# Kernel tuning notes

Hardware: AMD Instinct MI355X
Metric: run time of the kernel (lower is better)

Reference implementation:

```python
import jax, jax.numpy as jnp
import numpy as np

D_MODEL = 1024
D_STATE = 16
BATCH = 16384
LN_EPS = 1e-5


def _linear_params(key, out_d, in_d):
    # torch nn.Linear default init: U(-1/sqrt(in_d), 1/sqrt(in_d))
    bound = 1.0 / np.sqrt(in_d)
    kw, kb = jax.random.split(key)
    W = jax.random.uniform(kw, (out_d, in_d), minval=-bound, maxval=bound, dtype=jnp.float32)
    b = jax.random.uniform(kb, (out_d,), minval=-bound, maxval=bound, dtype=jnp.float32)
    return W, b


def setup_inputs() -> dict:
    key = jax.random.key(0)
    k_x, k_b, k_c, k_dt, k_o = jax.random.split(key, 5)
    Wb, bb = _linear_params(k_b, D_STATE, D_MODEL)
    Wc, bc = _linear_params(k_c, D_STATE, D_MODEL)
    Wdt, bdt = _linear_params(k_dt, D_MODEL, D_MODEL)
    Wo, bo = _linear_params(k_o, D_MODEL, D_MODEL)
    return {
        "x": jax.random.normal(k_x, (BATCH, D_MODEL), dtype=jnp.float32),
        "gamma": jnp.ones((D_MODEL,), jnp.float32),   # LayerNorm weight
        "beta": jnp.zeros((D_MODEL,), jnp.float32),   # LayerNorm bias
        "Wb": Wb, "bb": bb,
        "Wc": Wc, "bc": bc,
        "Wdt": Wdt, "bdt": bdt,
        "D_skip": jnp.ones((D_MODEL,), jnp.float32),  # self.D parameter
        "Wo": Wo, "bo": bo,
    }


def reference(x, gamma, beta, Wb, bb, Wc, bc, Wdt, bdt, D_skip, Wo, bo):
    residual = x
    # LayerNorm
    mu = jnp.mean(x, axis=-1, keepdims=True)
    var = jnp.var(x, axis=-1, keepdims=True)
    xn = (x - mu) * jax.lax.rsqrt(var + LN_EPS) * gamma + beta  # (B, D)

    Bm = xn @ Wb.T + bb                     # (B, N)
    Cm = xn @ Wc.T + bc                     # (B, N)
    dt = jax.nn.softplus(xn @ Wdt.T + bdt)  # (B, D)
    # dA = exp(dt[...,None] * -exp(A_log)) is computed in the original but unused.

    # h = dt[:,:,None] * Bm[:,None,:] * xn[:,:,None]; y = (h * Cm[:,None,:]).sum(-1)
    # The N-reduction factors: sum_n Bm[b,n]*Cm[b,n] is d-independent.
    s = jnp.sum(Bm * Cm, axis=-1, keepdims=True)  # (B, 1)
    y = dt * xn * s + xn * D_skip                 # (B, D)

    y = y @ Wo.T + bo
    return y + residual  # dropout is identity at inference
```

## Files before the change

### kernel.cpp

```cpp
#include <hip/hip_runtime.h>
#include <math.h>

#define BATCH   16384
#define DMODEL  1024
#define KPACK   3072
#define KPHYS   2048
#define LN_EPS  1e-5f

typedef __bf16 bf16x8 __attribute__((ext_vector_type(8)));
typedef float  f32x4  __attribute__((ext_vector_type(4)));

static __device__ __forceinline__ unsigned short f2bf(float v) {
  union { float f; unsigned u; } c; c.f = v;
  unsigned r = c.u + 0x7fffu + ((c.u >> 16) & 1u);
  return (unsigned short)(r >> 16);
}
static __device__ __forceinline__ float bf2f(unsigned short h) {
  union { unsigned u; float f; } c; c.u = ((unsigned)h) << 16;
  return c.f;
}

static __device__ __forceinline__ void gload16(const void* g, void* l) {
  __builtin_amdgcn_global_load_lds(
      (const __attribute__((address_space(1))) void*)g,
      (__attribute__((address_space(3))) void*)l, 16, 0, 0);
}

#define S_BAR() __builtin_amdgcn_s_barrier()
#define LGKM0() do { asm volatile("s_waitcnt lgkmcnt(0)" ::: "memory"); \
                     __builtin_amdgcn_sched_barrier(0); } while (0)
#define VMC8()  do { asm volatile("s_waitcnt vmcnt(8)" ::: "memory"); \
                     __builtin_amdgcn_sched_barrier(0); } while (0)

__global__ __launch_bounds__(256) void pack_kernel(
    const float* __restrict__ Wdt, const float* __restrict__ Wo,
    const float* __restrict__ Wb, const float* __restrict__ Wc,
    unsigned short* __restrict__ WdtP, unsigned short* __restrict__ WoP,
    unsigned short* __restrict__ WbcP) {
  int r = blockIdx.x;
  const float* src;
  unsigned short* dst;
  if (r < 1024)      { src = Wdt + (size_t)r * 1024;        dst = WdtP + (size_t)r * KPHYS; }
  else if (r < 2048) { src = Wo  + (size_t)(r-1024) * 1024; dst = WoP  + (size_t)(r-1024) * KPHYS; }
  else if (r < 2064) { src = Wb  + (size_t)(r-2048) * 1024; dst = WbcP + (size_t)(r-2048) * KPHYS; }
  else               { src = Wc  + (size_t)(r-2064) * 1024; dst = WbcP + (size_t)(r-2064+16) * KPHYS; }
  int t = threadIdx.x;
  float4 v = ((const float4*)src)[t];
  ushort4 hs, ls; unsigned short h;
  h = f2bf(v.x); hs.x = h; ls.x = f2bf(v.x - bf2f(h));
  h = f2bf(v.y); hs.y = h; ls.y = f2bf(v.y - bf2f(h));
  h = f2bf(v.z); hs.z = h; ls.z = f2bf(v.z - bf2f(h));
  h = f2bf(v.w); hs.w = h; ls.w = f2bf(v.w - bf2f(h));
  ((ushort4*)dst)[t] = hs;
  ((ushort4*)(dst + 1024))[t] = ls;
}

__global__ __launch_bounds__(256) void ln_kernel(
    const float* __restrict__ x, const float* __restrict__ gamma,
    const float* __restrict__ beta, unsigned short* __restrict__ xnp) {
  const int row = blockIdx.x;
  const int tid = threadIdx.x;
  const float4* xr = (const float4*)(x + (size_t)row * DMODEL);
  float4 v = xr[tid];
  float s = v.x + v.y + v.z + v.w;
  float q = v.x * v.x + v.y * v.y + v.z * v.z + v.w * v.w;
#pragma unroll
  for (int m = 1; m < 64; m <<= 1) {
    s += __shfl_xor(s, m, 64);
    q += __shfl_xor(q, m, 64);
  }
  __shared__ float ws[4], wq[4];
  int w = tid >> 6, l = tid & 63;
  if (l == 0) { ws[w] = s; wq[w] = q; }
  __syncthreads();
  s = ws[0] + ws[1] + ws[2] + ws[3];
  q = wq[0] + wq[1] + wq[2] + wq[3];
  float mu = s * (1.0f / DMODEL);
  float var = q * (1.0f / DMODEL) - mu * mu;
  float rs = rsqrtf(var + LN_EPS);
  float4 g = ((const float4*)gamma)[tid];
  float4 b = ((const float4*)beta)[tid];
  float xn0 = (v.x - mu) * rs * g.x + b.x;
  float xn1 = (v.y - mu) * rs * g.y + b.y;
  float xn2 = (v.z - mu) * rs * g.z + b.z;
  float xn3 = (v.w - mu) * rs * g.w + b.w;
  ushort4 hs, ls; unsigned short h;
  h = f2bf(xn0); hs.x = h; ls.x = f2bf(xn0 - bf2f(h));
  h = f2bf(xn1); hs.y = h; ls.y = f2bf(xn1 - bf2f(h));
  h = f2bf(xn2); hs.z = h; ls.z = f2bf(xn2 - bf2f(h));
  h = f2bf(xn3); hs.w = h; ls.w = f2bf(xn3 - bf2f(h));
  unsigned short* dst = xnp + (size_t)row * KPHYS;
  ((ushort4*)dst)[tid] = hs;
  ((ushort4*)(dst + 1024))[tid] = ls;
}

__global__ __launch_bounds__(256) void bc_kernel(
    const unsigned short* __restrict__ XNP, const unsigned short* __restrict__ WbcP,
    const float* __restrict__ bb, const float* __restrict__ bcv, float* __restrict__ S) {
  __shared__ char smem[(64 + 32) * 128];
  char* sA = smem;
  char* sB = smem + 64 * 128;
  const int tid = threadIdx.x;
  const int l = tid & 63;
  const int w = tid >> 6;
  const int m0 = blockIdx.x * 64;
  f32x4 acc0 = {0.f, 0.f, 0.f, 0.f};
  f32x4 acc1 = {0.f, 0.f, 0.f, 0.f};
  for (int kt = 0; kt < KPACK; kt += 64) {
    int ksA = kt < 2048 ? kt : kt - 2048;
    int ksB = kt < 1024 ? kt : kt - 1024;
#pragma unroll
    for (int i = 0; i < 2; ++i) {
      int qq = i * 256 + tid;
      int row = qq >> 3, ch = qq & 7;
      gload16(XNP + (size_t)(m0 + row) * KPHYS + ksA + ((ch ^ (row & 7)) << 3),
              sA + (i * 256 + w * 64) * 16);
    }
    {
      int row = tid >> 3, ch = tid & 7;
      gload16(WbcP + (size_t)row * KPHYS + ksB + ((ch ^ (row & 7)) << 3),
              sB + (w * 64) * 16);
    }
    __syncthreads();
#pragma unroll
    for (int kk = 0; kk < 2; ++kk) {
      int cs = ((kk * 4 + (l >> 4)) ^ (l & 7)) * 16;
      bf16x8 a  = *(const bf16x8*)(sA + (w * 16 + (l & 15)) * 128 + cs);
      bf16x8 b0 = *(const bf16x8*)(sB + ((l & 15)) * 128 + cs);
      bf16x8 b1 = *(const bf16x8*)(sB + (16 + (l & 15)) * 128 + cs);
      acc0 = __builtin_amdgcn_mfma_f32_16x16x32_bf16(a, b0, acc0, 0, 0, 0);
      acc1 = __builtin_amdgcn_mfma_f32_16x16x32_bf16(a, b1, acc1, 0, 0, 0);
    }
    __syncthreads();
  }
  int c = l & 15;
#pragma unroll
  for (int j = 0; j < 4; ++j) {
    float bmv = acc0[j] + bb[c];
    float cmv = acc1[j] + bcv[c];
    float p = bmv * cmv;
    p += __shfl_xor(p, 1, 64);
    p += __shfl_xor(p, 2, 64);
    p += __shfl_xor(p, 4, 64);
    p += __shfl_xor(p, 8, 64);
    if (c == 0) S[m0 + w * 16 + (l >> 4) * 4 + j] = p;
  }
}

template <int EPI>
__global__ __launch_bounds__(512, 2) void gemm8_kernel(
    const unsigned short* __restrict__ Ag,
    const unsigned short* __restrict__ Bg,
    const float* __restrict__ e0,
    const float* __restrict__ e1,
    const float* __restrict__ S,
    unsigned short* __restrict__ YP,
    float* __restrict__ outf) {
  __shared__ char smem[131072];
  char* const bufA[2] = { smem, smem + 65536 };
  char* const bufB[2] = { smem + 32768, smem + 98304 };

  const int tid = threadIdx.x;
  const int l = tid & 63;
  const int w = tid >> 6;
  const int wm = w >> 2;
  const int wn = w & 3;

  const int bid = blockIdx.x;
  const int sid = (bid & 7) * 32 + (bid >> 3);
  const int m0 = (sid >> 2) * 256;
  const int n0 = (sid & 3) * 256;

  f32x4 acc[8][4];
#pragma unroll
  for (int a = 0; a < 8; ++a)
#pragma unroll
    for (int b = 0; b < 4; ++b) acc[a][b] = (f32x4){0.f, 0.f, 0.f, 0.f};

  auto STAGE = [&](int bufi, int kt) {
    const int ksA = kt < 2048 ? kt : kt - 2048;
    const int ksB = kt < 1024 ? kt : kt - 1024;
#pragma unroll
    for (int r = 0; r < 4; ++r) {
      int qq = r * 512 + tid;
      int row = qq >> 3, ch = qq & 7;
      gload16(Ag + (size_t)(m0 + row) * KPHYS + ksA + ((ch ^ (row & 7)) << 3),
              bufA[bufi] + (r * 512 + w * 64) * 16);
    }
#pragma unroll
    for (int r = 0; r < 4; ++r) {
      int qq = r * 512 + tid;
      int row = qq >> 3, ch = qq & 7;
      gload16(Bg + (size_t)(n0 + row) * KPHYS + ksB + ((ch ^ (row & 7)) << 3),
              bufB[bufi] + (r * 512 + w * 64) * 16);
    }
  };

  const int rbA = (wm * 128 + (l & 15)) * 128;
  const int rbB = (wn * 64 + (l & 15)) * 128;
  int cs[2];
  cs[0] = (((l >> 4)) ^ (l & 7)) * 16;
  cs[1] = ((4 + (l >> 4)) ^ (l & 7)) * 16;

  bf16x8 aF[4][2], bF[2][2][2];
  auto LDA = [&](int bufi, int qm) {
#pragma unroll
    for (int mi = 0; mi < 4; ++mi)
#pragma unroll
      for (int kk = 0; kk < 2; ++kk)
        aF[mi][kk] = *(const bf16x8*)(bufA[bufi] + rbA + qm * 8192 + mi * 2048 + cs[kk]);
  };
  auto LDB = [&](int bufi, int qn) {
#pragma unroll
    for (int ni = 0; ni < 2; ++ni)
#pragma unroll
      for (int kk = 0; kk < 2; ++kk)
        bF[qn][ni][kk] = *(const bf16x8*)(bufB[bufi] + rbB + qn * 4096 + ni * 2048 + cs[kk]);
  };
  auto MFMA = [&](int qm, int qn) {
    __builtin_amdgcn_s_setprio(1);
#pragma unroll
    for (int kk = 0; kk < 2; ++kk)
#pragma unroll
      for (int mi = 0; mi < 4; ++mi)
#pragma unroll
        for (int ni = 0; ni < 2; ++ni)
          acc[qm * 4 + mi][qn * 2 + ni] = __builtin_amdgcn_mfma_f32_16x16x32_bf16(
              aF[mi][kk], bF[qn][ni][kk], acc[qm * 4 + mi][qn * 2 + ni], 0, 0, 0);
    __builtin_amdgcn_s_setprio(0);
  };

  STAGE(0, 0);
  STAGE(1, 64);
  VMC8();
  S_BAR();

  for (int it = 0; it < 24; ++it) {
    const int ktA = it * 128;
    const int kt2 = (ktA + 128 <= KPACK - 64) ? ktA + 128 : KPACK - 64;
    const int kt3 = (ktA + 192 <= KPACK - 64) ? ktA + 192 : KPACK - 64;
    LDA(0, 0); LDB(0, 0);
    S_BAR(); LGKM0(); MFMA(0, 0); S_BAR();
    LDB(0, 1);
    S_BAR(); LGKM0(); MFMA(0, 1); S_BAR();
    LDA(0, 1);
    S_BAR(); LGKM0(); MFMA(1, 1); S_BAR();
    STAGE(0, kt2);
    S_BAR(); MFMA(1, 0); VMC8(); S_BAR();
    LDA(1, 0); LDB(1, 0);
    S_BAR(); LGKM0(); MFMA(0, 0); S_BAR();
    LDB(1, 1);
    S_BAR(); LGKM0(); MFMA(0, 1); S_BAR();
    LDA(1, 1);
    S_BAR(); LGKM0(); MFMA(1, 1); S_BAR();
    STAGE(1, kt3);
    S_BAR(); MFMA(1, 0); VMC8(); S_BAR();
  }

  if constexpr (EPI == 1) {
#pragma unroll
    for (int a = 0; a < 8; ++a) {
      int rw = m0 + wm * 128 + (a >> 2) * 64 + (a & 3) * 16 + (l >> 4) * 4;
#pragma unroll
      for (int j = 0; j < 4; ++j) {
        int r = rw + j;
        float sv = S[r];
        size_t base = (size_t)r * KPHYS;
#pragma unroll
        for (int b = 0; b < 4; ++b) {
          int col = n0 + wn * 64 + (b >> 1) * 32 + (b & 1) * 16 + (l & 15);
          float v = acc[a][b][j] + e0[col];
          float sp = fmaxf(v, 0.f) + __logf(1.f + __expf(-fabsf(v)));
          float xnv = bf2f(Ag[base + col]) + bf2f(Ag[base + 1024 + col]);
          float y = sp * xnv * sv + xnv * e1[col];
          unsigned short h = f2bf(y);
          YP[base + col] = h;
          YP[base + 1024 + col] = f2bf(y - bf2f(h));
        }
      }
    }
  } else {
#pragma unroll
    for (int a = 0; a < 8; ++a) {
      int rw = m0 + wm * 128 + (a >> 2) * 64 + (a & 3) * 16 + (l >> 4) * 4;
#pragma unroll
      for (int j = 0; j < 4; ++j) {
        int r = rw + j;
        size_t base = (size_t)r * DMODEL;
#pragma unroll
        for (int b = 0; b < 4; ++b) {
          int col = n0 + wn * 64 + (b >> 1) * 32 + (b & 1) * 16 + (l & 15);
          outf[base + col] = acc[a][b][j] + e0[col] + e1[base + col];
        }
      }
    }
  }
}

extern "C" void kernel_launch(void* const* d_in, const int* in_sizes, int n_in,
                              void* d_out, int out_size, void* d_ws, size_t ws_size,
                              hipStream_t stream) {
  const float* x = (const float*)d_in[0];
  const float* gamma = (const float*)d_in[1];
  const float* beta = (const float*)d_in[2];
  const float* Wb = (const float*)d_in[3];
  const float* bb = (const float*)d_in[4];
  const float* Wc = (const float*)d_in[5];
  const float* bc = (const float*)d_in[6];
  const float* Wdt = (const float*)d_in[7];
  const float* bdt = (const float*)d_in[8];
  const float* Dsk = (const float*)d_in[9];
  const float* Wo = (const float*)d_in[10];
  const float* bo = (const float*)d_in[11];
  float* out = (float*)d_out;

  char* ws = (char*)d_ws;
  size_t off = 0;
  auto alloc = [&](size_t bytes) {
    char* p = ws + off;
    off = (off + bytes + 255) & ~(size_t)255;
    return p;
  };
  unsigned short* XNP  = (unsigned short*)alloc((size_t)BATCH * KPHYS * 2);
  unsigned short* YP   = (unsigned short*)alloc((size_t)BATCH * KPHYS * 2);
  unsigned short* WdtP = (unsigned short*)alloc((size_t)DMODEL * KPHYS * 2);
  unsigned short* WoP  = (unsigned short*)alloc((size_t)DMODEL * KPHYS * 2);
  unsigned short* WbcP = (unsigned short*)alloc((size_t)32 * KPHYS * 2);
  float* S = (float*)alloc((size_t)BATCH * 4);

  pack_kernel<<<2080, 256, 0, stream>>>(Wdt, Wo, Wb, Wc, WdtP, WoP, WbcP);
  ln_kernel<<<BATCH, 256, 0, stream>>>(x, gamma, beta, XNP);
  bc_kernel<<<BATCH / 64, 256, 0, stream>>>(XNP, WbcP, bb, bc, S);
  gemm8_kernel<1><<<256, 512, 0, stream>>>(XNP, WdtP, bdt, Dsk, S, YP, nullptr);
  gemm8_kernel<2><<<256, 512, 0, stream>>>(YP, WoP, bo, x, nullptr, nullptr, out);
}
```

Measured before the change: 384.6 us.

## Replace fine-grained quadrant MFMA schedule with per-buffer k-half tiles and fewer barriers

Replaces the 8-phase ping-pong schedule, which had many workgroup barriers and lgkm waits between quadrant MFMA groups, with a simpler per-buffer loop. Each buffer now runs two k-halves, each loading all A and B fragments then issuing 32 MFMAs, followed by one barrier before restaging. The epilogue row and column mapping is updated to match the new accumulator indexing. This cuts barrier overhead and lets the compiler schedule LDS reads freely. The trade-off is less interleaving of LDS reads and global staging with MFMA, plus more live fragment registers.

After: 369.2 us. 1.04x faster.

```diff
diff --git a/kernel.cpp b/kernel.cpp
--- a/kernel.cpp
+++ b/kernel.cpp
@@ -26,11 +26,12 @@
       (__attribute__((address_space(3))) void*)l, 16, 0, 0);
 }
 
-#define S_BAR() __builtin_amdgcn_s_barrier()
-#define LGKM0() do { asm volatile("s_waitcnt lgkmcnt(0)" ::: "memory"); \
-                     __builtin_amdgcn_sched_barrier(0); } while (0)
-#define VMC8()  do { asm volatile("s_waitcnt vmcnt(8)" ::: "memory"); \
-                     __builtin_amdgcn_sched_barrier(0); } while (0)
+#define SCHED0() __builtin_amdgcn_sched_barrier(0)
+#define MFENCE() asm volatile("" ::: "memory")
+#define SBAR_F() do { MFENCE(); __builtin_amdgcn_s_barrier(); MFENCE(); } while (0)
+#define VMC8()   do { asm volatile("s_waitcnt vmcnt(8)" ::: "memory"); } while (0)
+#define LGKM0_PIN() do { asm volatile("s_waitcnt lgkmcnt(0)" ::: "memory"); \
+                         __builtin_amdgcn_sched_barrier(0); } while (0)
 
 __global__ __launch_bounds__(256) void pack_kernel(
     const float* __restrict__ Wdt, const float* __restrict__ Wo,
@@ -202,65 +203,56 @@
   cs[0] = (((l >> 4)) ^ (l & 7)) * 16;
   cs[1] = ((4 + (l >> 4)) ^ (l & 7)) * 16;
 
-  bf16x8 aF[4][2], bF[2][2][2];
-  auto LDA = [&](int bufi, int qm) {
-#pragma unroll
-    for (int mi = 0; mi < 4; ++mi)
-#pragma unroll
-      for (int kk = 0; kk < 2; ++kk)
-        aF[mi][kk] = *(const bf16x8*)(bufA[bufi] + rbA + qm * 8192 + mi * 2048 + cs[kk]);
-  };
-  auto LDB = [&](int bufi, int qn) {
-#pragma unroll
-    for (int ni = 0; ni < 2; ++ni)
-#pragma unroll
-      for (int kk = 0; kk < 2; ++kk)
-        bF[qn][ni][kk] = *(const bf16x8*)(bufB[bufi] + rbB + qn * 4096 + ni * 2048 + cs[kk]);
-  };
-  auto MFMA = [&](int qm, int qn) {
+  auto TILEH = [&](int bufi, int kcs) {
+    bf16x8 fA[8], fB[4];
+#pragma unroll
+    for (int r = 0; r < 8; ++r)
+      fA[r] = *(const bf16x8*)(bufA[bufi] + rbA + r * 2048 + kcs);
+#pragma unroll
+    for (int c = 0; c < 4; ++c)
+      fB[c] = *(const bf16x8*)(bufB[bufi] + rbB + c * 2048 + kcs);
     __builtin_amdgcn_s_setprio(1);
 #pragma unroll
-    for (int kk = 0; kk < 2; ++kk)
-#pragma unroll
-      for (int mi = 0; mi < 4; ++mi)
-#pragma unroll
-        for (int ni = 0; ni < 2; ++ni)
-          acc[qm * 4 + mi][qn * 2 + ni] = __builtin_amdgcn_mfma_f32_16x16x32_bf16(
-              aF[mi][kk], bF[qn][ni][kk], acc[qm * 4 + mi][qn * 2 + ni], 0, 0, 0);
+    for (int r = 0; r < 8; ++r)
+#pragma unroll
+      for (int c = 0; c < 4; ++c)
+        acc[r][c] = __builtin_amdgcn_mfma_f32_16x16x32_bf16(
+            fA[r], fB[c], acc[r][c], 0, 0, 0);
     __builtin_amdgcn_s_setprio(0);
   };
+  auto TILE = [&](int bufi) {
+    TILEH(bufi, cs[0]);
+    SCHED0();
+    TILEH(bufi, cs[1]);
+  };
 
   STAGE(0, 0);
+  MFENCE();
   STAGE(1, 64);
   VMC8();
-  S_BAR();
+  SBAR_F();
 
   for (int it = 0; it < 24; ++it) {
-    const int ktA = it * 128;
-    const int kt2 = (ktA + 128 <= KPACK - 64) ? ktA + 128 : KPACK - 64;
-    const int kt3 = (ktA + 192 <= KPACK - 64) ? ktA + 192 : KPACK - 64;
-    LDA(0, 0); LDB(0, 0);
-    S_BAR(); LGKM0(); MFMA(0, 0); S_BAR();
-    LDB(0, 1);
-    S_BAR(); LGKM0(); MFMA(0, 1); S_BAR();
-    LDA(0, 1);
-    S_BAR(); LGKM0(); MFMA(1, 1); S_BAR();
+    const int kt2 = (it * 128 + 128 <= KPACK - 64) ? it * 128 + 128 : KPACK - 64;
+    const int kt3 = (it * 128 + 192 <= KPACK - 64) ? it * 128 + 192 : KPACK - 64;
+    TILE(0);
+    LGKM0_PIN();
+    SBAR_F();
     STAGE(0, kt2);
-    S_BAR(); MFMA(1, 0); VMC8(); S_BAR();
-    LDA(1, 0); LDB(1, 0);
-    S_BAR(); LGKM0(); MFMA(0, 0); S_BAR();
-    LDB(1, 1);
-    S_BAR(); LGKM0(); MFMA(0, 1); S_BAR();
-    LDA(1, 1);
-    S_BAR(); LGKM0(); MFMA(1, 1); S_BAR();
+    VMC8();
+    SBAR_F();
+    TILE(1);
+    LGKM0_PIN();
+    SBAR_F();
     STAGE(1, kt3);
-    S_BAR(); MFMA(1, 0); VMC8(); S_BAR();
+    VMC8();
+    SBAR_F();
   }
 
   if constexpr (EPI == 1) {
 #pragma unroll
     for (int a = 0; a < 8; ++a) {
-      int rw = m0 + wm * 128 + (a >> 2) * 64 + (a & 3) * 16 + (l >> 4) * 4;
+      int rw = m0 + wm * 128 + a * 16 + (l >> 4) * 4;
 #pragma unroll
       for (int j = 0; j < 4; ++j) {
         int r = rw + j;
@@ -268,7 +260,7 @@
         size_t base = (size_t)r * KPHYS;
 #pragma unroll
         for (int b = 0; b < 4; ++b) {
-          int col = n0 + wn * 64 + (b >> 1) * 32 + (b & 1) * 16 + (l & 15);
+          int col = n0 + wn * 64 + b * 16 + (l & 15);
           float v = acc[a][b][j] + e0[col];
           float sp = fmaxf(v, 0.f) + __logf(1.f + __expf(-fabsf(v)));
           float xnv = bf2f(Ag[base + col]) + bf2f(Ag[base + 1024 + col]);
@@ -282,14 +274,14 @@
   } else {
 #pragma unroll
     for (int a = 0; a < 8; ++a) {
-      int rw = m0 + wm * 128 + (a >> 2) * 64 + (a & 3) * 16 + (l >> 4) * 4;
+      int rw = m0 + wm * 128 + a * 16 + (l >> 4) * 4;
 #pragma unroll
       for (int j = 0; j < 4; ++j) {
         int r = rw + j;
         size_t base = (size_t)r * DMODEL;
 #pragma unroll
         for (int b = 0; b < 4; ++b) {
-          int col = n0 + wn * 64 + (b >> 1) * 32 + (b & 1) * 16 + (l & 15);
+          int col = n0 + wn * 64 + b * 16 + (l & 15);
           outf[base + col] = acc[a][b][j] + e0[col] + e1[base + col];
         }
       }
```
